# Performance work log

Measured on AMD Instinct MI355X. Metric: run time of the kernel, lower is better.

Reference implementation:

```python
import jax, jax.numpy as jnp
import numpy as np

N_HEADS = 32
N_KV_HEADS = 8
HEAD_DIM = 64
ROPE_BASE = 10000.0


def _rope(t):
    # t: [b, s, h, d]; Llama-style rotate-half RoPE
    b, s, h, d = t.shape
    inv_freq = 1.0 / (ROPE_BASE ** (jnp.arange(0, d, 2, dtype=jnp.float32) / d))
    freqs = jnp.arange(s, dtype=jnp.float32)[:, None] * inv_freq[None, :]  # [s, d/2]
    cos = jnp.cos(freqs)[None, :, None, :].astype(t.dtype)
    sin = jnp.sin(freqs)[None, :, None, :].astype(t.dtype)
    t1, t2 = t[..., : d // 2], t[..., d // 2 :]
    return jnp.concatenate([t1 * cos - t2 * sin, t2 * cos + t1 * sin], axis=-1)


def setup_inputs() -> dict:
    key = jax.random.key(0)
    ks = jax.random.split(key, 5)
    b, s, d = 2, 2048, 2048
    dkv = d // (N_HEADS // N_KV_HEADS)
    sc = 1.0 / np.sqrt(d)
    return {
        "x": jax.random.normal(ks[0], (b, s, d), jnp.float32),
        "wq": jax.random.normal(ks[1], (d, d), jnp.float32) * sc,
        "wk": jax.random.normal(ks[2], (d, dkv), jnp.float32) * sc,
        "wv": jax.random.normal(ks[3], (d, dkv), jnp.float32) * sc,
        "wo": jax.random.normal(ks[4], (d, d), jnp.float32) * sc,
    }


def reference(x, wq, wk, wv, wo):
    b, s, d = x.shape
    g = N_HEADS // N_KV_HEADS
    q = (x @ wq).reshape(b, s, N_HEADS, HEAD_DIM)
    k = (x @ wk).reshape(b, s, N_KV_HEADS, HEAD_DIM)
    v = (x @ wv).reshape(b, s, N_KV_HEADS, HEAD_DIM)
    q = _rope(q)
    k = _rope(k)
    # GQA: repeat kv heads to match query heads
    k = jnp.repeat(k, g, axis=2)  # [b, s, N_HEADS, d_h]
    v = jnp.repeat(v, g, axis=2)
    scale = 1.0 / np.sqrt(HEAD_DIM)
    scores = jnp.einsum("bqhd,bkhd->bhqk", q, k) * scale  # [b, h, s, s]
    causal = jnp.tril(jnp.ones((s, s), dtype=bool))
    scores = jnp.where(causal[None, None], scores, jnp.finfo(scores.dtype).min)
    probs = jax.nn.softmax(scores, axis=-1)
    out = jnp.einsum("bhqk,bkhd->bqhd", probs, v).reshape(b, s, d)
    return out @ wo
```

## Files before the change

kernel.cpp:

```cpp
#include <hip/hip_runtime.h>
#include <hip/hip_bf16.h>
#include <stdint.h>

typedef __attribute__((ext_vector_type(8))) __bf16 bf16x8;
typedef __attribute__((ext_vector_type(4))) __bf16 bf16x4;
typedef __attribute__((ext_vector_type(4))) float f32x4;

#define QSCALE (0.125f * 1.44269504f)

#define GL16(src, dst) __builtin_amdgcn_global_load_lds( \
    (const __attribute__((address_space(1))) void*)(src), \
    (__attribute__((address_space(3))) void*)(dst), 16, 0, 0)

static __device__ inline unsigned pkbf(float a, float b) {
  __bf16 x = (__bf16)a, y = (__bf16)b;
  unsigned short ux = __builtin_bit_cast(unsigned short, x);
  unsigned short uy = __builtin_bit_cast(unsigned short, y);
  return ((unsigned)uy << 16) | ux;
}

static __device__ inline float ex2(float x) {
#if __has_builtin(__builtin_amdgcn_exp2f)
  return __builtin_amdgcn_exp2f(x);
#else
  float r;
  asm("v_exp_f32 %0, %1" : "=v"(r) : "v"(x));
  return r;
#endif
}

__global__ void k_cvt(const float* __restrict__ in, __bf16* __restrict__ out, int n8) {
  int i = blockIdx.x * blockDim.x + threadIdx.x;
  if (i >= n8) return;
  const float4* p = (const float4*)(in) + (size_t)i * 2;
  float4 a = p[0], b = p[1];
  bf16x8 o;
  o[0] = (__bf16)a.x; o[1] = (__bf16)a.y; o[2] = (__bf16)a.z; o[3] = (__bf16)a.w;
  o[4] = (__bf16)b.x; o[5] = (__bf16)b.y; o[6] = (__bf16)b.z; o[7] = (__bf16)b.w;
  ((bf16x8*)out)[i] = o;
}

__global__ void k_tconv(const float* __restrict__ w, __bf16* __restrict__ wT, int K, int N) {
  __shared__ float tile[32][33];
  int n0 = blockIdx.x * 32, k0 = blockIdx.y * 32;
  int tx = threadIdx.x, ty = threadIdx.y;
#pragma unroll
  for (int i = 0; i < 32; i += 8)
    tile[ty + i][tx] = w[(size_t)(k0 + ty + i) * N + n0 + tx];
  __syncthreads();
#pragma unroll
  for (int i = 0; i < 32; i += 8)
    wT[(size_t)(n0 + ty + i) * K + k0 + tx] = (__bf16)tile[tx][ty + i];
}

__global__ void k_ropetab(float* __restrict__ ct, float* __restrict__ st) {
  int i = blockIdx.x * blockDim.x + threadIdx.x;
  if (i >= 2048 * 32) return;
  int s = i >> 5, j = i & 31;
  float invf = powf(10000.0f, -(float)j / 32.0f);
  float fr = (float)s * invf;
  ct[i] = cosf(fr);
  st[i] = sinf(fr);
}

template <int BN, int NW, int WPN, int MODE>
__global__ __launch_bounds__(NW * 64, NW / 4) void k_gemm256(const __bf16* __restrict__ A,
                                                             const __bf16* __restrict__ BT,
                                                             void* __restrict__ C0,
                                                             __bf16* __restrict__ kb,
                                                             __bf16* __restrict__ vt,
                                                             const float* __restrict__ ct,
                                                             const float* __restrict__ st,
                                                             int K, int NBN) {
  constexpr int WPM = NW / WPN;
  constexpr int MF = 256 / WPM / 16;
  constexpr int NF = BN / WPN / 16;
  constexpr int MH = MF / 2;
  constexpr int CHA = 256 * 8;
  constexpr int CHB = BN * 8;
  constexpr int PA = CHA / (NW * 64);
  constexpr int RA = CHA - PA * NW * 64;
  constexpr int PB = CHB / (NW * 64);
  static_assert(CHB % (NW * 64) == 0, "B chunks must tile threads");
  static_assert(RA % 64 == 0, "A remainder must be wave-aligned");
  static_assert(NF == 4, "epilogue assumes 64-col wave window");
  __shared__ __align__(16) __bf16 lA[2][256 * 64];
  __shared__ __align__(16) __bf16 lB[2][BN * 64];
  int bm = (blockIdx.x / NBN) << 8;
  int bn = (blockIdx.x % NBN) * BN;
  int tid = threadIdx.x, l = tid & 63, w = tid >> 6;
  int wr = w / WPN, wc = w % WPN;
  int lrow = l & 15, lk = l >> 4;
  int NT = K >> 6;
  f32x4 acc[MF][NF] = {};

#define STG(T, BUF)                                                           \
  do {                                                                        \
    int k0_ = (T) << 6;                                                       \
    _Pragma("unroll") for (int i_ = 0; i_ < PA; i_++) {                       \
      int ch_ = i_ * (NW * 64) + tid;                                         \
      int r_ = ch_ >> 3, c_ = ch_ & 7;                                        \
      GL16(A + (size_t)(bm + r_) * K + k0_ + ((c_ ^ (r_ & 7)) << 3),          \
           &lA[BUF][(i_ * (NW * 64) + (w << 6)) * 8]);                        \
    }                                                                         \
    if constexpr (RA > 0) {                                                   \
      if (tid < RA) {                                                         \
        int ch_ = PA * (NW * 64) + tid;                                       \
        int r_ = ch_ >> 3, c_ = ch_ & 7;                                      \
        GL16(A + (size_t)(bm + r_) * K + k0_ + ((c_ ^ (r_ & 7)) << 3),        \
             &lA[BUF][(PA * (NW * 64) + (w << 6)) * 8]);                      \
      }                                                                       \
    }                                                                         \
    _Pragma("unroll") for (int i_ = 0; i_ < PB; i_++) {                       \
      int ch_ = i_ * (NW * 64) + tid;                                         \
      int r_ = ch_ >> 3, c_ = ch_ & 7;                                        \
      GL16(BT + (size_t)(bn + r_) * K + k0_ + ((c_ ^ (r_ & 7)) << 3),         \
           &lB[BUF][(i_ * (NW * 64) + (w << 6)) * 8]);                        \
    }                                                                         \
  } while (0)

#define WAITN()                                                               \
  do {                                                                        \
    if constexpr (RA > 0) {                                                   \
      if (w < (RA >> 6))                                                      \
        asm volatile("s_waitcnt vmcnt(%0)" ::"i"(PA + PB + 1) : "memory");    \
      else                                                                    \
        asm volatile("s_waitcnt vmcnt(%0)" ::"i"(PA + PB) : "memory");        \
    } else {                                                                  \
      asm volatile("s_waitcnt vmcnt(%0)" ::"i"(PA + PB) : "memory");          \
    }                                                                         \
  } while (0)

  STG(0, 0);
  STG(1, 1);
  WAITN();
  __builtin_amdgcn_sched_barrier(0);
  __builtin_amdgcn_s_barrier();

  for (int t = 0; t < NT; t++) {
    int buf = t & 1;
    const char* bA = (const char*)lA[buf];
    const char* bB = (const char*)lB[buf];
    bf16x8 bfr[NF][2], af0[MH][2], af1[MH][2];
#pragma unroll
    for (int nf = 0; nf < NF; nf++) {
      int row = wc * (NF * 16) + nf * 16 + lrow;
#pragma unroll
      for (int kc = 0; kc < 2; kc++)
        bfr[nf][kc] = *(const bf16x8*)(bB + row * 128 +
                                       ((kc * 64 + 16 * lk) ^ ((row & 7) << 4)));
    }
#pragma unroll
    for (int mf = 0; mf < MH; mf++) {
      int row = wr * (MF * 16) + mf * 16 + lrow;
#pragma unroll
      for (int kc = 0; kc < 2; kc++)
        af0[mf][kc] = *(const bf16x8*)(bA + row * 128 +
                                       ((kc * 64 + 16 * lk) ^ ((row & 7) << 4)));
    }
    __builtin_amdgcn_s_setprio(1);
#pragma unroll
    for (int kc = 0; kc < 2; kc++)
#pragma unroll
      for (int mf = 0; mf < MH; mf++)
#pragma unroll
        for (int nf = 0; nf < NF; nf++)
          acc[mf][nf] = __builtin_amdgcn_mfma_f32_16x16x32_bf16(af0[mf][kc], bfr[nf][kc],
                                                                acc[mf][nf], 0, 0, 0);
    __builtin_amdgcn_s_setprio(0);
#pragma unroll
    for (int mf = 0; mf < MH; mf++) {
      int row = wr * (MF * 16) + (MH + mf) * 16 + lrow;
#pragma unroll
      for (int kc = 0; kc < 2; kc++)
        af1[mf][kc] = *(const bf16x8*)(bA + row * 128 +
                                       ((kc * 64 + 16 * lk) ^ ((row & 7) << 4)));
    }
    asm volatile("s_waitcnt lgkmcnt(0)" ::: "memory");
    __builtin_amdgcn_sched_barrier(0);
    __builtin_amdgcn_s_barrier();
    if (t + 2 < NT) STG(t + 2, buf);
    __builtin_amdgcn_s_setprio(1);
#pragma unroll
    for (int kc = 0; kc < 2; kc++)
#pragma unroll
      for (int mf = 0; mf < MH; mf++)
#pragma unroll
        for (int nf = 0; nf < NF; nf++)
          acc[MH + mf][nf] = __builtin_amdgcn_mfma_f32_16x16x32_bf16(
              af1[mf][kc], bfr[nf][kc], acc[MH + mf][nf], 0, 0, 0);
    __builtin_amdgcn_s_setprio(0);
    if (t + 2 < NT) {
      WAITN();
    } else {
      asm volatile("s_waitcnt vmcnt(0)" ::: "memory");
    }
    __builtin_amdgcn_sched_barrier(0);
    __builtin_amdgcn_s_barrier();
  }
#undef STG
#undef WAITN

  if constexpr (MODE == 0) {
    int wcb = bn + wc * 64;
    __bf16* qb = (__bf16*)C0;
    if (wcb < 2048) {
#pragma unroll
      for (int mf = 0; mf < MF; mf++)
#pragma unroll
        for (int r = 0; r < 4; r++) {
          int row = bm + wr * (MF * 16) + mf * 16 + 4 * lk + r;
          int sidx = row & 2047;
#pragma unroll
          for (int nfl = 0; nfl < 2; nfl++) {
            int d = nfl * 16 + lrow;
            float c = ct[sidx * 32 + d], sn = st[sidx * 32 + d];
            float a = acc[mf][nfl][r], b2 = acc[mf][nfl + 2][r];
            qb[(size_t)row * 2048 + wcb + d] = (__bf16)((a * c - b2 * sn) * QSCALE);
            qb[(size_t)row * 2048 + wcb + d + 32] = (__bf16)((b2 * c + a * sn) * QSCALE);
          }
        }
    } else if (wcb < 2560) {
      int cb = wcb - 2048;
#pragma unroll
      for (int mf = 0; mf < MF; mf++)
#pragma unroll
        for (int r = 0; r < 4; r++) {
          int row = bm + wr * (MF * 16) + mf * 16 + 4 * lk + r;
          int sidx = row & 2047;
#pragma unroll
          for (int nfl = 0; nfl < 2; nfl++) {
            int d = nfl * 16 + lrow;
            float c = ct[sidx * 32 + d], sn = st[sidx * 32 + d];
            float a = acc[mf][nfl][r], b2 = acc[mf][nfl + 2][r];
            kb[(size_t)row * 512 + cb + d] = (__bf16)(a * c - b2 * sn);
            kb[(size_t)row * 512 + cb + d + 32] = (__bf16)(b2 * c + a * sn);
          }
        }
    } else {
      int hkk = (wcb - 2560) >> 6;
#pragma unroll
      for (int mf = 0; mf < MF; mf++)
#pragma unroll
        for (int nf = 0; nf < NF; nf++)
#pragma unroll
          for (int r = 0; r < 4; r++) {
            int row = bm + wr * (MF * 16) + mf * 16 + 4 * lk + r;
            int dd = nf * 16 + lrow;
            int bb = row >> 11, s = row & 2047;
            vt[(size_t)(((bb << 3) + hkk) * 64 + dd) * 2048 + s] = (__bf16)acc[mf][nf][r];
          }
    }
  } else {
    float* C = (float*)C0;
#pragma unroll
    for (int mf = 0; mf < MF; mf++)
#pragma unroll
      for (int nf = 0; nf < NF; nf++)
#pragma unroll
        for (int r = 0; r < 4; r++) {
          int row = bm + wr * (MF * 16) + mf * 16 + 4 * lk + r;
          int col = bn + wc * 64 + nf * 16 + lrow;
          C[(size_t)row * 2048 + col] = acc[mf][nf][r];
        }
  }
}

__global__ __launch_bounds__(256, 3) void k_attn(const __bf16* __restrict__ Q,
                                                 const __bf16* __restrict__ Kb,
                                                 const __bf16* __restrict__ VT,
                                                 __bf16* __restrict__ O) {
  __shared__ __align__(16) __bf16 lK[2][64 * 64];
  __shared__ __align__(16) __bf16 lV[2][64 * 64];
  int bid = blockIdx.x;
  int c = 63 - (bid >> 4);
  int hk = bid & 7;
  int b = (bid >> 3) & 1;
  int tid = threadIdx.x, l = tid & 63, w = tid >> 6;
  int h = hk * 4 + w;
  int lrow = l & 15, lk = l >> 4;
  int sw = (lrow & 7) << 4;
  int tl = c >> 1;

#define STAGE(BUF, T)                                                                     \
  do {                                                                                    \
    int kv0_ = (T) * 64;                                                                  \
    _Pragma("unroll") for (int i_ = 0; i_ < 2; i_++) {                                    \
      int cb_ = i_ * 256 + w * 64;                                                        \
      int chunk_ = cb_ + l;                                                               \
      int row_ = chunk_ >> 3, cc_ = chunk_ & 7;                                           \
      GL16(Kb + (size_t)(b * 2048 + kv0_ + row_) * 512 + hk * 64 +                        \
               ((cc_ ^ (row_ & 7)) << 3),                                                 \
           &lK[BUF][cb_ * 8]);                                                            \
      GL16(VT + (size_t)((b * 8 + hk) * 64 + row_) * 2048 + kv0_ +                        \
               ((cc_ ^ (row_ & 7)) << 3),                                                 \
           &lV[BUF][cb_ * 8]);                                                            \
    }                                                                                     \
  } while (0)

  bf16x8 aq[2][2];
#pragma unroll
  for (int qf = 0; qf < 2; qf++) {
    int qrow = c * 32 + qf * 16 + lrow;
    const __bf16* qp = Q + (size_t)(b * 2048 + qrow) * 2048 + h * 64 + lk * 8;
    aq[qf][0] = *(const bf16x8*)qp;
    aq[qf][1] = *(const bf16x8*)(qp + 32);
  }
  f32x4 o[2][4] = {};
  float lp[2] = {0.f, 0.f};
  STAGE(0, 0);
  for (int t = 0, buf = 0; t <= tl; t++, buf ^= 1) {
    asm volatile("s_waitcnt vmcnt(0)" ::: "memory");
    __syncthreads();
    if (t < tl) STAGE(buf ^ 1, t + 1);
    const char* K_ = (const char*)lK[buf];
    const char* V_ = (const char*)lV[buf];
    f32x4 s4[2][4];
#pragma unroll
    for (int nf = 0; nf < 4; nf++) {
      const char* kr = K_ + (nf * 16 + lrow) * 128;
      bf16x8 bk0 = *(const bf16x8*)(kr + ((16 * lk) ^ sw));
      bf16x8 bk1 = *(const bf16x8*)(kr + ((64 + 16 * lk) ^ sw));
#pragma unroll
      for (int qf = 0; qf < 2; qf++) {
        f32x4 z = {};
        z = __builtin_amdgcn_mfma_f32_16x16x32_bf16(bk0, aq[qf][0], z, 0, 0, 0);
        z = __builtin_amdgcn_mfma_f32_16x16x32_bf16(bk1, aq[qf][1], z, 0, 0, 0);
        s4[qf][nf] = z;
      }
    }
    if (t == tl) {
      int qo = (c & 1) * 32;
#pragma unroll
      for (int qf = 0; qf < 2; qf++) {
        int qoff = qo + qf * 16 + lrow;
#pragma unroll
        for (int nf = 0; nf < 4; nf++)
#pragma unroll
          for (int r = 0; r < 4; r++)
            if (nf * 16 + 4 * lk + r > qoff) s4[qf][nf][r] = -1e30f;
      }
    }
#pragma unroll
    for (int qf = 0; qf < 2; qf++) {
      float ps = 0.f;
#pragma unroll
      for (int nf = 0; nf < 4; nf++)
#pragma unroll
        for (int r = 0; r < 4; r++) {
          float pv = ex2(s4[qf][nf][r]);
          s4[qf][nf][r] = pv;
          ps += pv;
        }
      lp[qf] += ps;
    }
#pragma unroll
    for (int np = 0; np < 2; np++) {
      bf16x8 pb[2];
#pragma unroll
      for (int qf = 0; qf < 2; qf++) {
        uint4 t4;
        t4.x = pkbf(s4[qf][np][0], s4[qf][np][1]);
        t4.y = pkbf(s4[qf][np][2], s4[qf][np][3]);
        t4.z = pkbf(s4[qf][np + 2][0], s4[qf][np + 2][1]);
        t4.w = pkbf(s4[qf][np + 2][2], s4[qf][np + 2][3]);
        pb[qf] = __builtin_bit_cast(bf16x8, t4);
      }
#pragma unroll
      for (int dn = 0; dn < 4; dn++) {
        const char* vr = V_ + (dn * 16 + lrow) * 128;
        uint2 a0 = *(const uint2*)(vr + ((np * 32 + 8 * lk) ^ sw));
        uint2 a1 = *(const uint2*)(vr + (((np + 2) * 32 + 8 * lk) ^ sw));
        uint4 av;
        av.x = a0.x; av.y = a0.y; av.z = a1.x; av.w = a1.y;
        bf16x8 va = __builtin_bit_cast(bf16x8, av);
#pragma unroll
        for (int qf = 0; qf < 2; qf++)
          o[qf][dn] = __builtin_amdgcn_mfma_f32_16x16x32_bf16(va, pb[qf], o[qf][dn], 0, 0, 0);
      }
    }
  }
#pragma unroll
  for (int qf = 0; qf < 2; qf++) {
    float s = lp[qf];
    s += __shfl_xor(s, 16);
    s += __shfl_xor(s, 32);
    float inv = 1.f / s;
    int qrow = c * 32 + qf * 16 + lrow;
    __bf16* op = O + (size_t)(b * 2048 + qrow) * 2048 + h * 64 + 4 * lk;
#pragma unroll
    for (int dn = 0; dn < 4; dn++) {
      bf16x4 stv;
#pragma unroll
      for (int r = 0; r < 4; r++) stv[r] = (__bf16)(o[qf][dn][r] * inv);
      *(bf16x4*)(op + dn * 16) = stv;
    }
  }
#undef STAGE
}

extern "C" void kernel_launch(void* const* d_in, const int* in_sizes, int n_in,
                              void* d_out, int out_size, void* d_ws, size_t ws_size,
                              hipStream_t stream) {
  const float* x = (const float*)d_in[0];
  const float* wq = (const float*)d_in[1];
  const float* wk = (const float*)d_in[2];
  const float* wv = (const float*)d_in[3];
  const float* wo = (const float*)d_in[4];
  char* ws = (char*)d_ws;
  __bf16* xb    = (__bf16*)(ws + 0);
  __bf16* wqkvT = (__bf16*)(ws + 16777216);
  __bf16* woT   = (__bf16*)(ws + 29360128);
  __bf16* qb    = (__bf16*)(ws + 37748736);
  __bf16* kb    = (__bf16*)(ws + 54525952);
  __bf16* vt    = (__bf16*)(ws + 58720256);
  __bf16* ob    = (__bf16*)(ws + 62914560);
  float*  ct    = (float*)(ws + 79691776);
  float*  st    = (float*)(ws + 79953920);
  float* out = (float*)d_out;

  k_cvt<<<4096, 256, 0, stream>>>(x, xb, 1048576);
  k_tconv<<<dim3(64, 64), dim3(32, 8), 0, stream>>>(wq, wqkvT, 2048, 2048);
  k_tconv<<<dim3(16, 64), dim3(32, 8), 0, stream>>>(wk, wqkvT + (size_t)2048 * 2048, 2048, 512);
  k_tconv<<<dim3(16, 64), dim3(32, 8), 0, stream>>>(wv, wqkvT + (size_t)2560 * 2048, 2048, 512);
  k_tconv<<<dim3(64, 64), dim3(32, 8), 0, stream>>>(wo, woT, 2048, 2048);
  k_ropetab<<<256, 256, 0, stream>>>(ct, st);
  k_gemm256<192, 12, 3, 0><<<256, 768, 0, stream>>>(xb, wqkvT, qb, kb, vt, ct, st, 2048, 16);
  k_attn<<<1024, 256, 0, stream>>>(qb, kb, vt, ob);
  k_gemm256<128, 8, 2, 1><<<256, 512, 0, stream>>>(ob, woT, out, nullptr, nullptr, nullptr,
                                                   nullptr, 2048, 16);
}
```

Measured before the change: 171.6 us.

## Triple-buffer A tiles in GEMM mainloop and swizzle block order

Moves the A operand to a three-stage LDS ring that prefetches three k-tiles ahead, while B stays double-buffered. vmcnt waits are recomputed for the steady and tail phases. All A fragment LDS reads are hoisted before the first MFMA half so the mid-loop barrier no longer waits on them. Block indices are remapped with an interleave of 8 to change which tiles run concurrently for L2 reuse. The extra A buffer raises LDS use and may reduce occupancy, and the hoisted reads raise register pressure.

```diff
diff --git a/kernel.cpp b/kernel.cpp
--- a/kernel.cpp
+++ b/kernel.cpp
@@ -84,17 +84,24 @@
   static_assert(CHB % (NW * 64) == 0, "B chunks must tile threads");
   static_assert(RA % 64 == 0, "A remainder must be wave-aligned");
   static_assert(NF == 4, "epilogue assumes 64-col wave window");
-  __shared__ __align__(16) __bf16 lA[2][256 * 64];
+  constexpr int LB = PB;
+  constexpr int LA0 = PA + (RA > 0 ? 1 : 0);
+  constexpr int LA1 = PA;
+  constexpr int NS0 = 2 * LA0 + LB, NS1 = 2 * LA1 + LB;
+  constexpr int NM0 = LA0 + LB, NM1 = LA1 + LB;
+  __shared__ __align__(16) __bf16 lA[3][256 * 64];
   __shared__ __align__(16) __bf16 lB[2][BN * 64];
-  int bm = (blockIdx.x / NBN) << 8;
-  int bn = (blockIdx.x % NBN) * BN;
+  int bid = blockIdx.x;
+  int lg = (bid & 7) * ((int)gridDim.x >> 3) + (bid >> 3);
+  int bm = (lg / NBN) << 8;
+  int bn = (lg % NBN) * BN;
   int tid = threadIdx.x, l = tid & 63, w = tid >> 6;
   int wr = w / WPN, wc = w % WPN;
   int lrow = l & 15, lk = l >> 4;
   int NT = K >> 6;
   f32x4 acc[MF][NF] = {};
 
-#define STG(T, BUF)                                                           \
+#define STGA(T, BUF)                                                          \
   do {                                                                        \
     int k0_ = (T) << 6;                                                       \
     _Pragma("unroll") for (int i_ = 0; i_ < PA; i_++) {                       \
@@ -111,6 +118,11 @@
              &lA[BUF][(PA * (NW * 64) + (w << 6)) * 8]);                      \
       }                                                                       \
     }                                                                         \
+  } while (0)
+
+#define STGB(T, BUF)                                                          \
+  do {                                                                        \
+    int k0_ = (T) << 6;                                                       \
     _Pragma("unroll") for (int i_ = 0; i_ < PB; i_++) {                       \
       int ch_ = i_ * (NW * 64) + tid;                                         \
       int r_ = ch_ >> 3, c_ = ch_ & 7;                                        \
@@ -119,28 +131,41 @@
     }                                                                         \
   } while (0)
 
-#define WAITN()                                                               \
+#define WAIT_STEADY()                                                         \
   do {                                                                        \
     if constexpr (RA > 0) {                                                   \
       if (w < (RA >> 6))                                                      \
-        asm volatile("s_waitcnt vmcnt(%0)" ::"i"(PA + PB + 1) : "memory");    \
+        asm volatile("s_waitcnt vmcnt(%0)" ::"i"(NS0) : "memory");            \
       else                                                                    \
-        asm volatile("s_waitcnt vmcnt(%0)" ::"i"(PA + PB) : "memory");        \
+        asm volatile("s_waitcnt vmcnt(%0)" ::"i"(NS1) : "memory");            \
     } else {                                                                  \
-      asm volatile("s_waitcnt vmcnt(%0)" ::"i"(PA + PB) : "memory");          \
+      asm volatile("s_waitcnt vmcnt(%0)" ::"i"(NS1) : "memory");              \
     }                                                                         \
   } while (0)
 
-  STG(0, 0);
-  STG(1, 1);
-  WAITN();
+#define WAIT_MID()                                                            \
+  do {                                                                        \
+    if constexpr (RA > 0) {                                                   \
+      if (w < (RA >> 6))                                                      \
+        asm volatile("s_waitcnt vmcnt(%0)" ::"i"(NM0) : "memory");            \
+      else                                                                    \
+        asm volatile("s_waitcnt vmcnt(%0)" ::"i"(NM1) : "memory");            \
+    } else {                                                                  \
+      asm volatile("s_waitcnt vmcnt(%0)" ::"i"(NM1) : "memory");              \
+    }                                                                         \
+  } while (0)
+
+  STGB(0, 0); STGA(0, 0);
+  STGB(1, 1); STGA(1, 1);
+  STGA(2, 2);
+  WAIT_STEADY();
   __builtin_amdgcn_sched_barrier(0);
   __builtin_amdgcn_s_barrier();
 
+  int a0 = 0;
   for (int t = 0; t < NT; t++) {
-    int buf = t & 1;
-    const char* bA = (const char*)lA[buf];
-    const char* bB = (const char*)lB[buf];
+    const char* bA = (const char*)lA[a0];
+    const char* bB = (const char*)lB[t & 1];
     bf16x8 bfr[NF][2], af0[MH][2], af1[MH][2];
 #pragma unroll
     for (int nf = 0; nf < NF; nf++) {
@@ -156,6 +181,14 @@
 #pragma unroll
       for (int kc = 0; kc < 2; kc++)
         af0[mf][kc] = *(const bf16x8*)(bA + row * 128 +
+                                       ((kc * 64 + 16 * lk) ^ ((row & 7) << 4)));
+    }
+#pragma unroll
+    for (int mf = 0; mf < MH; mf++) {
+      int row = wr * (MF * 16) + (MH + mf) * 16 + lrow;
+#pragma unroll
+      for (int kc = 0; kc < 2; kc++)
+        af1[mf][kc] = *(const bf16x8*)(bA + row * 128 +
                                        ((kc * 64 + 16 * lk) ^ ((row & 7) << 4)));
     }
     __builtin_amdgcn_s_setprio(1);
@@ -168,18 +201,11 @@
           acc[mf][nf] = __builtin_amdgcn_mfma_f32_16x16x32_bf16(af0[mf][kc], bfr[nf][kc],
                                                                 acc[mf][nf], 0, 0, 0);
     __builtin_amdgcn_s_setprio(0);
-#pragma unroll
-    for (int mf = 0; mf < MH; mf++) {
-      int row = wr * (MF * 16) + (MH + mf) * 16 + lrow;
-#pragma unroll
-      for (int kc = 0; kc < 2; kc++)
-        af1[mf][kc] = *(const bf16x8*)(bA + row * 128 +
-                                       ((kc * 64 + 16 * lk) ^ ((row & 7) << 4)));
-    }
     asm volatile("s_waitcnt lgkmcnt(0)" ::: "memory");
     __builtin_amdgcn_sched_barrier(0);
     __builtin_amdgcn_s_barrier();
-    if (t + 2 < NT) STG(t + 2, buf);
+    if (t + 2 < NT) STGB(t + 2, t & 1);
+    if (t + 3 < NT) STGA(t + 3, a0);
     __builtin_amdgcn_s_setprio(1);
 #pragma unroll
     for (int kc = 0; kc < 2; kc++)
@@ -190,16 +216,21 @@
           acc[MH + mf][nf] = __builtin_amdgcn_mfma_f32_16x16x32_bf16(
               af1[mf][kc], bfr[nf][kc], acc[MH + mf][nf], 0, 0, 0);
     __builtin_amdgcn_s_setprio(0);
-    if (t + 2 < NT) {
-      WAITN();
-    } else {
+    if (t + 3 < NT) {
+      WAIT_STEADY();
+    } else if (t + 2 < NT) {
+      WAIT_MID();
+    } else if (t + 1 < NT) {
       asm volatile("s_waitcnt vmcnt(0)" ::: "memory");
     }
     __builtin_amdgcn_sched_barrier(0);
     __builtin_amdgcn_s_barrier();
+    a0 = (a0 == 2) ? 0 : a0 + 1;
   }
-#undef STG
-#undef WAITN
+#undef STGA
+#undef STGB
+#undef WAIT_STEADY
+#undef WAIT_MID
 
   if constexpr (MODE == 0) {
     int wcb = bn + wc * 64;
```

New measurement: 168.7 us. Within noise of the previous version (-1.7%).

## Double attention query tile to 64 rows per wave to reuse K/V tiles

Applied to the files above, without the earlier changes.

Each attention block now handles 64 query rows per head (four 16-row fragments per wave) instead of 32, halving the grid to 512 blocks. K fragments are loaded from LDS once per KV tile and reused across all four query fragments, and each staged K/V tile serves twice as many queries, cutting global and LDS traffic per query. The cost is more accumulator registers (occupancy hint lowered from 3 to 2 waves per SIMD), fewer blocks to balance the causal triangle, and a coarser diagonal tile handled by masking.

```diff
diff --git a/kernel.cpp b/kernel.cpp
--- a/kernel.cpp
+++ b/kernel.cpp
@@ -266,21 +266,21 @@
   }
 }
 
-__global__ __launch_bounds__(256, 3) void k_attn(const __bf16* __restrict__ Q,
+__global__ __launch_bounds__(256, 2) void k_attn(const __bf16* __restrict__ Q,
                                                  const __bf16* __restrict__ Kb,
                                                  const __bf16* __restrict__ VT,
                                                  __bf16* __restrict__ O) {
   __shared__ __align__(16) __bf16 lK[2][64 * 64];
   __shared__ __align__(16) __bf16 lV[2][64 * 64];
   int bid = blockIdx.x;
-  int c = 63 - (bid >> 4);
+  int c = 31 - (bid >> 4);
   int hk = bid & 7;
   int b = (bid >> 3) & 1;
   int tid = threadIdx.x, l = tid & 63, w = tid >> 6;
   int h = hk * 4 + w;
   int lrow = l & 15, lk = l >> 4;
   int sw = (lrow & 7) << 4;
-  int tl = c >> 1;
+  int tl = c;
 
 #define STAGE(BUF, T)                                                                     \
   do {                                                                                    \
@@ -298,16 +298,16 @@
     }                                                                                     \
   } while (0)
 
-  bf16x8 aq[2][2];
-#pragma unroll
-  for (int qf = 0; qf < 2; qf++) {
-    int qrow = c * 32 + qf * 16 + lrow;
+  bf16x8 aq[4][2];
+#pragma unroll
+  for (int qf = 0; qf < 4; qf++) {
+    int qrow = c * 64 + qf * 16 + lrow;
     const __bf16* qp = Q + (size_t)(b * 2048 + qrow) * 2048 + h * 64 + lk * 8;
     aq[qf][0] = *(const bf16x8*)qp;
     aq[qf][1] = *(const bf16x8*)(qp + 32);
   }
-  f32x4 o[2][4] = {};
-  float lp[2] = {0.f, 0.f};
+  f32x4 o[4][4] = {};
+  float lp[4] = {0.f, 0.f, 0.f, 0.f};
   STAGE(0, 0);
   for (int t = 0, buf = 0; t <= tl; t++, buf ^= 1) {
     asm volatile("s_waitcnt vmcnt(0)" ::: "memory");
@@ -315,78 +315,85 @@
     if (t < tl) STAGE(buf ^ 1, t + 1);
     const char* K_ = (const char*)lK[buf];
     const char* V_ = (const char*)lV[buf];
-    f32x4 s4[2][4];
+    bf16x8 bk[4][2];
 #pragma unroll
     for (int nf = 0; nf < 4; nf++) {
       const char* kr = K_ + (nf * 16 + lrow) * 128;
-      bf16x8 bk0 = *(const bf16x8*)(kr + ((16 * lk) ^ sw));
-      bf16x8 bk1 = *(const bf16x8*)(kr + ((64 + 16 * lk) ^ sw));
-#pragma unroll
-      for (int qf = 0; qf < 2; qf++) {
-        f32x4 z = {};
-        z = __builtin_amdgcn_mfma_f32_16x16x32_bf16(bk0, aq[qf][0], z, 0, 0, 0);
-        z = __builtin_amdgcn_mfma_f32_16x16x32_bf16(bk1, aq[qf][1], z, 0, 0, 0);
-        s4[qf][nf] = z;
+      bk[nf][0] = *(const bf16x8*)(kr + ((16 * lk) ^ sw));
+      bk[nf][1] = *(const bf16x8*)(kr + ((64 + 16 * lk) ^ sw));
+    }
+#pragma unroll
+    for (int qp2 = 0; qp2 < 2; qp2++) {
+      f32x4 s4[2][4];
+#pragma unroll
+      for (int nf = 0; nf < 4; nf++)
+#pragma unroll
+        for (int q2 = 0; q2 < 2; q2++) {
+          int qf = qp2 * 2 + q2;
+          f32x4 z = {};
+          z = __builtin_amdgcn_mfma_f32_16x16x32_bf16(bk[nf][0], aq[qf][0], z, 0, 0, 0);
+          z = __builtin_amdgcn_mfma_f32_16x16x32_bf16(bk[nf][1], aq[qf][1], z, 0, 0, 0);
+          s4[q2][nf] = z;
+        }
+      if (t == tl) {
+#pragma unroll
+        for (int q2 = 0; q2 < 2; q2++) {
+          int qoff = (qp2 * 2 + q2) * 16 + lrow;
+#pragma unroll
+          for (int nf = 0; nf < 4; nf++)
+#pragma unroll
+            for (int r = 0; r < 4; r++)
+              if (nf * 16 + 4 * lk + r > qoff) s4[q2][nf][r] = -1e30f;
+        }
       }
-    }
-    if (t == tl) {
-      int qo = (c & 1) * 32;
-#pragma unroll
-      for (int qf = 0; qf < 2; qf++) {
-        int qoff = qo + qf * 16 + lrow;
+#pragma unroll
+      for (int q2 = 0; q2 < 2; q2++) {
+        float ps = 0.f;
 #pragma unroll
         for (int nf = 0; nf < 4; nf++)
 #pragma unroll
-          for (int r = 0; r < 4; r++)
-            if (nf * 16 + 4 * lk + r > qoff) s4[qf][nf][r] = -1e30f;
+          for (int r = 0; r < 4; r++) {
+            float pv = ex2(s4[q2][nf][r]);
+            s4[q2][nf][r] = pv;
+            ps += pv;
+          }
+        lp[qp2 * 2 + q2] += ps;
       }
-    }
-#pragma unroll
-    for (int qf = 0; qf < 2; qf++) {
-      float ps = 0.f;
-#pragma unroll
-      for (int nf = 0; nf < 4; nf++)
-#pragma unroll
-        for (int r = 0; r < 4; r++) {
-          float pv = ex2(s4[qf][nf][r]);
-          s4[qf][nf][r] = pv;
-          ps += pv;
-        }
-      lp[qf] += ps;
-    }
-#pragma unroll
-    for (int np = 0; np < 2; np++) {
-      bf16x8 pb[2];
-#pragma unroll
-      for (int qf = 0; qf < 2; qf++) {
-        uint4 t4;
-        t4.x = pkbf(s4[qf][np][0], s4[qf][np][1]);
-        t4.y = pkbf(s4[qf][np][2], s4[qf][np][3]);
-        t4.z = pkbf(s4[qf][np + 2][0], s4[qf][np + 2][1]);
-        t4.w = pkbf(s4[qf][np + 2][2], s4[qf][np + 2][3]);
-        pb[qf] = __builtin_bit_cast(bf16x8, t4);
+#pragma unroll
+      for (int np = 0; np < 2; np++) {
+        bf16x8 pb[2];
+#pragma unroll
+        for (int q2 = 0; q2 < 2; q2++) {
+          uint4 t4;
+          t4.x = pkbf(s4[q2][np][0], s4[q2][np][1]);
+          t4.y = pkbf(s4[q2][np][2], s4[q2][np][3]);
+          t4.z = pkbf(s4[q2][np + 2][0], s4[q2][np + 2][1]);
+          t4.w = pkbf(s4[q2][np + 2][2], s4[q2][np + 2][3]);
+          pb[q2] = __builtin_bit_cast(bf16x8, t4);
+        }
+#pragma unroll
+        for (int dn = 0; dn < 4; dn++) {
+          const char* vr = V_ + (dn * 16 + lrow) * 128;
+          uint2 a0 = *(const uint2*)(vr + ((np * 32 + 8 * lk) ^ sw));
+          uint2 a1 = *(const uint2*)(vr + (((np + 2) * 32 + 8 * lk) ^ sw));
+          uint4 av;
+          av.x = a0.x; av.y = a0.y; av.z = a1.x; av.w = a1.y;
+          bf16x8 va = __builtin_bit_cast(bf16x8, av);
+#pragma unroll
+          for (int q2 = 0; q2 < 2; q2++)
+            o[qp2 * 2 + q2][dn] =
+                __builtin_amdgcn_mfma_f32_16x16x32_bf16(va, pb[q2], o[qp2 * 2 + q2][dn], 0, 0, 0);
+        }
       }
-#pragma unroll
-      for (int dn = 0; dn < 4; dn++) {
-        const char* vr = V_ + (dn * 16 + lrow) * 128;
-        uint2 a0 = *(const uint2*)(vr + ((np * 32 + 8 * lk) ^ sw));
-        uint2 a1 = *(const uint2*)(vr + (((np + 2) * 32 + 8 * lk) ^ sw));
-        uint4 av;
-        av.x = a0.x; av.y = a0.y; av.z = a1.x; av.w = a1.y;
-        bf16x8 va = __builtin_bit_cast(bf16x8, av);
-#pragma unroll
-        for (int qf = 0; qf < 2; qf++)
-          o[qf][dn] = __builtin_amdgcn_mfma_f32_16x16x32_bf16(va, pb[qf], o[qf][dn], 0, 0, 0);
-      }
     }
   }
 #pragma unroll
-  for (int qf = 0; qf < 2; qf++) {
+  for (int qf = 0; qf < 4; qf++) {
     float s = lp[qf];
     s += __shfl_xor(s, 16);
     s += __shfl_xor(s, 32);
     float inv = 1.f / s;
-    int qrow = c * 32 + qf * 16 + lrow;
+    int qrow = c * 64 + qf * 16 + lrow;
     __bf16* op = O + (size_t)(b * 2048 + qrow) * 2048 + h * 64 + 4 * lk;
 #pragma unroll
     for (int dn = 0; dn < 4; dn++) {
@@ -426,7 +433,7 @@
   k_tconv<<<dim3(64, 64), dim3(32, 8), 0, stream>>>(wo, woT, 2048, 2048);
   k_ropetab<<<256, 256, 0, stream>>>(ct, st);
   k_gemm256<192, 12, 3, 0><<<256, 768, 0, stream>>>(xb, wqkvT, qb, kb, vt, ct, st, 2048, 16);
-  k_attn<<<1024, 256, 0, stream>>>(qb, kb, vt, ob);
+  k_attn<<<512, 256, 0, stream>>>(qb, kb, vt, ob);
   k_gemm256<128, 8, 2, 1><<<256, 512, 0, stream>>>(ob, woT, out, nullptr, nullptr, nullptr,
                                                    nullptr, 2048, 16);
 }
```

Result: slower. 182.3 us (+6.2%).
